# Optimization experiments

Measured on AMD Instinct MI355X. Metric: run time of the kernel, lower is better.

## Reference

```python
import jax, jax.numpy as jnp
import numpy as np

EPS = 1e-8       # module epsilon for L1 renormalize
LN_EPS = 1e-5    # torch LayerNorm default eps
NUM_ITER = 3
TEMP = 1.0


def _ln(x, g, b):
    m = x.mean(-1, keepdims=True)
    v = ((x - m) ** 2).mean(-1, keepdims=True)
    return (x - m) * jax.lax.rsqrt(v + LN_EPS) * g + b


def _gru(x, h, W_ih, W_hh, b_ih, b_hh):
    # torch GRUCell: r,z,n gate ordering
    gx = x @ W_ih.T + b_ih
    gh = h @ W_hh.T + b_hh
    xr, xz, xn = jnp.split(gx, 3, axis=-1)
    hr, hz, hn = jnp.split(gh, 3, axis=-1)
    r = jax.nn.sigmoid(xr + hr)
    z = jax.nn.sigmoid(xz + hz)
    n = jnp.tanh(xn + r * hn)
    return (1.0 - z) * n + z * h


def setup_inputs() -> dict:
    key = jax.random.key(0)
    ks = jax.random.split(key, 12)
    B, T, C, S, D, H = 32, 4096, 256, 8, 256, 512

    def xav(k, shape):
        fan_out, fan_in = shape
        lim = (6.0 / (fan_in + fan_out)) ** 0.5
        return jax.random.uniform(k, shape, jnp.float32, -lim, lim)

    return dict(
        inputs=jax.random.normal(ks[0], (B, T, C), jnp.float32),
        slots=jax.random.normal(ks[1], (B, S, D), jnp.float32),
        ln_in_g=jnp.ones((C,), jnp.float32), ln_in_b=jnp.zeros((C,), jnp.float32),
        ln_s_g=jnp.ones((D,), jnp.float32), ln_s_b=jnp.zeros((D,), jnp.float32),
        ln_m_g=jnp.ones((D,), jnp.float32), ln_m_b=jnp.zeros((D,), jnp.float32),
        Wq=xav(ks[2], (D, D)), Wk=xav(ks[3], (D, C)), Wv=xav(ks[4], (D, C)),
        W_ih=xav(ks[5], (3 * D, D)), W_hh=xav(ks[6], (3 * D, D)),
        b_ih=jnp.zeros((3 * D,), jnp.float32), b_hh=jnp.zeros((3 * D,), jnp.float32),
        W1=xav(ks[7], (H, D)), b1=jnp.zeros((H,), jnp.float32),
        W2=xav(ks[8], (D, H)), b2=jnp.zeros((D,), jnp.float32),
    )


def reference(inputs, slots, ln_in_g, ln_in_b, ln_s_g, ln_s_b, ln_m_g, ln_m_b,
              Wq, Wk, Wv, W_ih, W_hh, b_ih, b_hh, W1, b1, W2, b2):
    D = slots.shape[-1]
    x = _ln(inputs, ln_in_g, ln_in_b)           # [B,T,C]
    k = x @ Wk.T                                # [B,T,D]
    v = x @ Wv.T                                # [B,T,D]
    scale = D ** (-0.5)
    logits = attn_sw = None
    for _ in range(NUM_ITER):
        slots_prev = slots
        s = _ln(slots, ln_s_g, ln_s_b)
        q = (s @ Wq.T) * scale                  # [B,S,D]
        logits = jnp.einsum('bsd,btd->bst', q, k)
        attn = jax.nn.softmax(logits / TEMP, axis=1)   # softmax over slots
        a = attn + EPS
        attn_sw = a / a.sum(-1, keepdims=True)         # L1 renorm over tokens
        updates = jnp.einsum('bst,btd->bsd', attn_sw, v)
        slots = _gru(updates, slots_prev, W_ih, W_hh, b_ih, b_hh)
        slots = slots + (jax.nn.relu(_ln(slots, ln_m_g, ln_m_b) @ W1.T + b1) @ W2.T + b2)
    return slots, logits, attn_sw
```

## Files before the change

kernel.cpp:

```cpp
#include <hip/hip_runtime.h>
#include <cstdint>
#include <cstddef>

typedef __bf16 bf16;
typedef float  f32x4  __attribute__((ext_vector_type(4)));
typedef __bf16 bf16x8 __attribute__((ext_vector_type(8)));
typedef __bf16 bf16x4 __attribute__((ext_vector_type(4)));

__global__ __launch_bounds__(256) void k_prep1(
    const float* __restrict__ slots_in, const float* __restrict__ W1,
    const float* __restrict__ W2,
    float* __restrict__ slots, bf16* __restrict__ W1T, bf16* __restrict__ W2T)
{
    const int i = blockIdx.x * 256 + threadIdx.x;
    if      (i <  65536) { slots[i] = slots_in[i]; }
    else if (i < 196608) { int j = i -  65536; int k = j >> 9, c = j & 511;
                           W1T[j] = (bf16)W1[c*256 + k]; }
    else if (i < 327680) { int j = i - 196608; int k = j >> 8, c = j & 255;
                           W2T[j] = (bf16)W2[c*512 + k]; }
}

__global__ __launch_bounds__(256) void k_prep2(
    const float* __restrict__ Wq, const float* __restrict__ Wk,
    const float* __restrict__ W_ih, const float* __restrict__ Wv,
    bf16* __restrict__ Mqk, float* __restrict__ Wxg)
{
    const int c = threadIdx.x;
    __shared__ float v[256];
    if (blockIdx.x < 256) {
        const int e = blockIdx.x;
        v[c] = Wq[(size_t)c*256 + e];
        __syncthreads();
        float a = 0.f;
#pragma unroll 8
        for (int d = 0; d < 256; ++d) a += v[d] * Wk[(size_t)d*256 + c];
        Mqk[(size_t)e*256 + c] = (bf16)(a * 0.0625f);
    } else {
        const int g = blockIdx.x - 256;
        v[c] = W_ih[(size_t)g*256 + c];
        __syncthreads();
        float a = 0.f;
#pragma unroll 8
        for (int d = 0; d < 256; ++d) a += v[d] * Wv[(size_t)d*256 + c];
        Wxg[(size_t)g*256 + c] = a;
    }
}

__global__ __launch_bounds__(256) void k_prep3(
    const float* __restrict__ Wxg, const float* __restrict__ W_hh,
    bf16* __restrict__ WgT)
{
    const int j = blockIdx.x * 256 + threadIdx.x;
    const int k = j / 1536, col = j - k*1536;
    WgT[j] = (bf16)((col < 768) ? Wxg[(size_t)col*256 + k] : W_hh[(size_t)(col-768)*256 + k]);
}

__global__ __launch_bounds__(256) void k_ln_in(
    const float* __restrict__ x, const float* __restrict__ g,
    const float* __restrict__ b, bf16* __restrict__ xln)
{
    const int wave = threadIdx.x >> 6, lane = threadIdx.x & 63;
    const size_t row = (size_t)blockIdx.x * 4 + wave;
    const float* xr = x + row * 256 + lane * 4;
    f32x4 v = *(const f32x4*)xr;
    float s  = v[0] + v[1] + v[2] + v[3];
    float ss = v[0]*v[0] + v[1]*v[1] + v[2]*v[2] + v[3]*v[3];
#pragma unroll
    for (int m = 32; m >= 1; m >>= 1) { s += __shfl_xor(s, m); ss += __shfl_xor(ss, m); }
    const float mean = s * (1.f/256.f);
    const float var  = ss * (1.f/256.f) - mean*mean;
    const float rstd = rsqrtf(var + 1e-5f);
    const f32x4 gg = *(const f32x4*)(g + lane*4);
    const f32x4 bb = *(const f32x4*)(b + lane*4);
    bf16x4 o;
#pragma unroll
    for (int e = 0; e < 4; ++e) o[e] = (bf16)((v[e]-mean)*rstd*gg[e] + bb[e]);
    *(bf16x4*)(xln + row*256 + lane*4) = o;
}

__global__ __launch_bounds__(256) void k_tr(
    const bf16* __restrict__ xln, bf16* __restrict__ xlnT)
{
    const int tt = blockIdx.x, ct = blockIdx.y, b = blockIdx.z;
    const int tid = threadIdx.x;
    __shared__ __align__(16) char tile[64*128];
    {
        const int row = tid >> 2, cq = (tid & 3) * 16;
        const bf16* src = xln + ((size_t)(b*4096 + tt*64 + row))*256 + ct*64 + cq;
        bf16x8 v0 = *(const bf16x8*)src;
        bf16x8 v1 = *(const bf16x8*)(src + 8);
        const int swz = (row & 7) << 4;
        *(bf16x8*)(tile + row*128 + ((cq*2)      ^ swz)) = v0;
        *(bf16x8*)(tile + row*128 + ((cq*2 + 16) ^ swz)) = v1;
    }
    __syncthreads();
    {
        const int c = tid & 63, tq = tid >> 6;
        bf16 val[16];
#pragma unroll
        for (int j = 0; j < 16; ++j) {
            const int t = tq*16 + j;
            val[j] = *(const bf16*)(tile + t*128 + ((2*c) ^ ((t & 7) << 4)));
        }
        bf16* dst = xlnT + ((size_t)(b*256 + ct*64 + c))*4096 + tt*64 + tq*16;
        *(bf16x8*)dst       = *(bf16x8*)&val[0];
        *(bf16x8*)(dst + 8) = *(bf16x8*)&val[8];
    }
}

__device__ __forceinline__ void gemv8(const bf16* __restrict__ wp, int LDW,
                                      const float* __restrict__ sp, int klen4,
                                      float* __restrict__ ac)
{
#pragma unroll 8
    for (int k4 = 0; k4 < klen4; ++k4) {
        const f32x4 sv = *(const f32x4*)(sp + k4*4);
#pragma unroll
        for (int kk = 0; kk < 4; ++kk) {
            const bf16x8 w = *(const bf16x8*)(wp + (size_t)(k4*4+kk)*LDW);
#pragma unroll
            for (int j = 0; j < 8; ++j) ac[j] += sv[kk]*(float)w[j];
        }
    }
}

__global__ __launch_bounds__(256) void k_q0(
    const float* __restrict__ slots, const bf16* __restrict__ Mqk,
    const float* __restrict__ g_s, const float* __restrict__ b_s,
    bf16* __restrict__ q2bf, float* __restrict__ den)
{
    const int bs = blockIdx.x, tid = threadIdx.x;
    __shared__ float sln[256], part[2048], red[8];
    const float v0 = slots[(size_t)bs*256 + tid];
    if (tid == 0) den[bs] = 0.f;
    {
        float s1 = v0, s2 = v0*v0;
#pragma unroll
        for (int m = 32; m >= 1; m >>= 1) { s1 += __shfl_xor(s1, m); s2 += __shfl_xor(s2, m); }
        if ((tid & 63) == 0) { red[tid >> 6] = s1; red[4 + (tid >> 6)] = s2; }
    }
    __syncthreads();
    {
        const float mean = (red[0]+red[1]+red[2]+red[3])*(1.f/256.f);
        const float var  = (red[4]+red[5]+red[6]+red[7])*(1.f/256.f) - mean*mean;
        const float rstd = rsqrtf(var + 1e-5f);
        sln[tid] = (v0-mean)*rstd*g_s[tid] + b_s[tid];
    }
    __syncthreads();
    {
        const int g8 = tid & 31, ks = tid >> 5;
        float ac[8] = {0,0,0,0,0,0,0,0};
        gemv8(Mqk + (size_t)(ks*32)*256 + g8*8, 256, sln + ks*32, 8, ac);
#pragma unroll
        for (int j = 0; j < 8; ++j) part[ks*256 + g8*8 + j] = ac[j];
    }
    __syncthreads();
    {
        float a = 0.f;
#pragma unroll
        for (int k = 0; k < 8; ++k) a += part[k*256 + tid];
        q2bf[(size_t)bs*256 + tid] = (bf16)a;
    }
}

__global__ __launch_bounds__(256) void k_attn1(
    const bf16* __restrict__ xln, const bf16* __restrict__ q2bf,
    bf16* __restrict__ abuf, float* __restrict__ den,
    float* __restrict__ logits_out, int write_logits)
{
    const int chunk = blockIdx.x, b = blockIdx.y;
    const int wv = threadIdx.x >> 6, lane = threadIdx.x & 63;
    const int sA = lane & 15;
    const int ko = (lane >> 4) * 8;

    bf16x8 aq[8];
    if (sA < 8) {
#pragma unroll
        for (int kk = 0; kk < 8; ++kk)
            aq[kk] = *(const bf16x8*)(q2bf + (size_t)(b*8 + sA)*256 + kk*32 + ko);
    } else {
#pragma unroll
        for (int kk = 0; kk < 8; ++kk) aq[kk] = (bf16x8){0,0,0,0,0,0,0,0};
    }

    float dacc[4] = {0.f, 0.f, 0.f, 0.f};
#pragma unroll
    for (int it = 0; it < 4; ++it) {
        const int t0 = chunk*256 + wv*64 + it*16;
        f32x4 acc = {0.f, 0.f, 0.f, 0.f};
        const bf16* xp = xln + (size_t)(b*4096 + t0 + sA)*256 + ko;
#pragma unroll
        for (int kk = 0; kk < 8; ++kk) {
            const bf16x8 bfr = *(const bf16x8*)(xp + kk*32);
            acc = __builtin_amdgcn_mfma_f32_16x16x32_bf16(aq[kk], bfr, acc, 0, 0, 0);
        }
        if (lane < 32) {
            float m1 = fmaxf(fmaxf(acc[0], acc[1]), fmaxf(acc[2], acc[3]));
            const float m2 = __shfl_xor(m1, 16);
            const float mx = fmaxf(m1, m2);
            float e[4], s4 = 0.f;
#pragma unroll
            for (int r = 0; r < 4; ++r) { e[r] = expf(acc[r] - mx); s4 += e[r]; }
            const float so = __shfl_xor(s4, 16);
            const float inv = 1.f / (s4 + so);
            const int t = t0 + (lane & 15);
            bf16x4 ab;
#pragma unroll
            for (int r = 0; r < 4; ++r) {
                const float av = e[r]*inv + 1e-8f;
                dacc[r] += av;
                ab[r] = (bf16)av;
            }
            *(bf16x4*)(abuf + (size_t)(b*4096 + t)*8 + (lane >> 4)*4) = ab;
            if (write_logits) {
#pragma unroll
                for (int r = 0; r < 4; ++r)
                    logits_out[(size_t)(b*8 + (lane >> 4)*4 + r)*4096 + t] = acc[r];
            }
        }
    }
    if (lane < 32) {
#pragma unroll
        for (int r = 0; r < 4; ++r) {
            float v = dacc[r];
            v += __shfl_xor(v, 1); v += __shfl_xor(v, 2);
            v += __shfl_xor(v, 4); v += __shfl_xor(v, 8);
            if ((lane & 15) == 0) atomicAdd(&den[b*8 + (lane >> 4)*4 + r], v);
        }
    }
}

__global__ __launch_bounds__(256) void k_attn2(
    const bf16* __restrict__ xlnT, const bf16* __restrict__ abuf,
    float* __restrict__ numpart)
{
    const int chunk = blockIdx.x, b = blockIdx.y, tid = threadIdx.x;
    const int wv = tid >> 6, lane = tid & 63;
    __shared__ __align__(16) bf16 aT[8][528];

#pragma unroll
    for (int r = 0; r < 2; ++r) {
        const int t = r*256 + tid;
        const bf16x8 a8 = *(const bf16x8*)(abuf + ((size_t)b*4096 + chunk*512 + t)*8);
#pragma unroll
        for (int s = 0; s < 8; ++s) aT[s][t] = a8[s];
    }
    __syncthreads();

    const int sA = lane & 15, ko = (lane >> 4) * 8;
    f32x4 acc[4] = {{0,0,0,0},{0,0,0,0},{0,0,0,0},{0,0,0,0}};
#pragma unroll 4
    for (int kt = 0; kt < 16; ++kt) {
        bf16x8 af;
        if (sA < 8) af = *(const bf16x8*)&aT[sA][kt*32 + ko];
        else        af = (bf16x8){0,0,0,0,0,0,0,0};
#pragma unroll
        for (int i = 0; i < 4; ++i) {
            const int c = (wv + i*4)*16 + sA;
            const bf16x8 bfr = *(const bf16x8*)(
                xlnT + ((size_t)(b*256 + c))*4096 + chunk*512 + kt*32 + ko);
            acc[i] = __builtin_amdgcn_mfma_f32_16x16x32_bf16(af, bfr, acc[i], 0, 0, 0);
        }
    }
    if (lane < 32) {
#pragma unroll
        for (int i = 0; i < 4; ++i) {
            const int c = (wv + i*4)*16 + (lane & 15);
#pragma unroll
            for (int r = 0; r < 4; ++r) {
                const int s = (lane >> 4)*4 + r;
                numpart[(((size_t)b*8 + chunk)*8 + s)*256 + c] = acc[i][r];
            }
        }
    }
}

__global__ __launch_bounds__(256) void k_attnsw(
    const float* __restrict__ logits, const float* __restrict__ den,
    float* __restrict__ attn_out)
{
    const int chunk = blockIdx.x, b = blockIdx.y;
    const int t = chunk*256 + threadIdx.x;
    float l[8];
#pragma unroll
    for (int s = 0; s < 8; ++s) l[s] = logits[(size_t)(b*8 + s)*4096 + t];
    float mx = l[0];
#pragma unroll
    for (int s = 1; s < 8; ++s) mx = fmaxf(mx, l[s]);
    float e[8], sum = 0.f;
#pragma unroll
    for (int s = 0; s < 8; ++s) { e[s] = expf(l[s] - mx); sum += e[s]; }
    const float inv = 1.f/sum;
#pragma unroll
    for (int s = 0; s < 8; ++s)
        attn_out[(size_t)(b*8 + s)*4096 + t] = (e[s]*inv + 1e-8f) / den[b*8 + s];
}

__global__ __launch_bounds__(512) void k_slot(
    const float* __restrict__ numpart, float* __restrict__ den,
    float* __restrict__ slots,
    const bf16* __restrict__ WgT,
    const float* __restrict__ b_ih, const float* __restrict__ b_hh,
    const float* __restrict__ g_m, const float* __restrict__ b_m,
    const bf16* __restrict__ W1T, const float* __restrict__ b1,
    const bf16* __restrict__ W2T, const float* __restrict__ b2,
    const bf16* __restrict__ Mqk,
    const float* __restrict__ g_s, const float* __restrict__ b_s,
    bf16* __restrict__ q2bf, float* __restrict__ out_slots, int last)
{
    const int bs = blockIdx.x, b = bs >> 3, s = bs & 7;
    const int tid = threadIdx.x;
    __shared__ float HS[256], ynd[256], G[1536], hpr[256];
    __shared__ float hln[256], hid[512], sln[256];
    __shared__ float part[4096];
    __shared__ float red[8];
    __shared__ float dsc;

    {
        const int h = tid >> 8, d2 = tid & 255;
        float a = 0.f;
        const float* np = numpart + (((size_t)b*8 + h*4)*8 + s)*256 + d2;
#pragma unroll
        for (int c = 0; c < 4; ++c) a += np[(size_t)c*2048];
        part[h*256 + d2] = a;
        if (tid < 256) HS[tid] = slots[(size_t)bs*256 + tid];
        if (tid == 0) { dsc = den[bs]; den[bs] = 0.f; }
    }
    __syncthreads();
    if (tid < 256) ynd[tid] = (part[tid] + part[256 + tid]) / dsc;
    __syncthreads();

    if (tid < 384) {
        const int g8 = tid % 192, ks = tid / 192;
        const int col = g8*8;
        const float* sp = ((col < 768) ? ynd : HS) + ks*128;
        float ac[8] = {0,0,0,0,0,0,0,0};
        gemv8(WgT + (size_t)(ks*128)*1536 + col, 1536, sp, 32, ac);
#pragma unroll
        for (int j = 0; j < 8; ++j) part[ks*1536 + col + j] = ac[j];
    }
    __syncthreads();
    for (int t = tid; t < 1536; t += 512) {
        const float bias = (t < 768) ? b_ih[t] : b_hh[t - 768];
        G[t] = part[t] + part[1536 + t] + bias;
    }
    __syncthreads();

    if (tid < 256) {
        const float r = 1.f/(1.f + expf(-(G[tid]       + G[768  + tid])));
        const float z = 1.f/(1.f + expf(-(G[256 + tid] + G[1024 + tid])));
        const float n = tanhf(G[512 + tid] + r*G[1280 + tid]);
        hpr[tid] = (1.f - z)*n + z*HS[tid];
    }
    __syncthreads();

    if (tid < 256) {
        const float v = hpr[tid];
        float s1 = v, s2 = v*v;
#pragma unroll
        for (int m = 32; m >= 1; m >>= 1) { s1 += __shfl_xor(s1, m); s2 += __shfl_xor(s2, m); }
        if ((tid & 63) == 0) { red[tid >> 6] = s1; red[4 + (tid >> 6)] = s2; }
    }
    __syncthreads();
    if (tid < 256) {
        const float mean = (red[0]+red[1]+red[2]+red[3])*(1.f/256.f);
        const float var  = (red[4]+red[5]+red[6]+red[7])*(1.f/256.f) - mean*mean;
        const float rstd = rsqrtf(var + 1e-5f);
        hln[tid] = (hpr[tid]-mean)*rstd*g_m[tid] + b_m[tid];
    }
    __syncthreads();

    {
        const int g8 = tid & 63, ks = tid >> 6;
        float ac[8] = {0,0,0,0,0,0,0,0};
        gemv8(W1T + (size_t)(ks*32)*512 + g8*8, 512, hln + ks*32, 8, ac);
#pragma unroll
        for (int j = 0; j < 8; ++j) part[ks*512 + g8*8 + j] = ac[j];
    }
    __syncthreads();
    {
        float a = b1[tid];
#pragma unroll
        for (int k = 0; k < 8; ++k) a += part[k*512 + tid];
        hid[tid] = fmaxf(a, 0.f);
    }
    __syncthreads();

    {
        const int g8 = tid & 31, ks = tid >> 5;
        float ac[8] = {0,0,0,0,0,0,0,0};
        gemv8(W2T + (size_t)(ks*32)*256 + g8*8, 256, hid + ks*32, 8, ac);
#pragma unroll
        for (int j = 0; j < 8; ++j) part[ks*256 + g8*8 + j] = ac[j];
    }
    __syncthreads();
    if (tid < 256) {
        float a = 0.f;
#pragma unroll
        for (int k = 0; k < 16; ++k) a += part[k*256 + tid];
        const float val = hpr[tid] + a + b2[tid];
        HS[tid] = val;
        slots[(size_t)bs*256 + tid] = val;
        if (last) out_slots[(size_t)bs*256 + tid] = val;
    }
    __syncthreads();
    if (last) return;

    if (tid < 256) {
        const float v = HS[tid];
        float s1 = v, s2 = v*v;
#pragma unroll
        for (int m = 32; m >= 1; m >>= 1) { s1 += __shfl_xor(s1, m); s2 += __shfl_xor(s2, m); }
        if ((tid & 63) == 0) { red[tid >> 6] = s1; red[4 + (tid >> 6)] = s2; }
    }
    __syncthreads();
    if (tid < 256) {
        const float mean = (red[0]+red[1]+red[2]+red[3])*(1.f/256.f);
        const float var  = (red[4]+red[5]+red[6]+red[7])*(1.f/256.f) - mean*mean;
        const float rstd = rsqrtf(var + 1e-5f);
        sln[tid] = (HS[tid]-mean)*rstd*g_s[tid] + b_s[tid];
    }
    __syncthreads();

    {
        const int g8 = tid & 31, ks = tid >> 5;
        float ac[8] = {0,0,0,0,0,0,0,0};
        gemv8(Mqk + (size_t)(ks*16)*256 + g8*8, 256, sln + ks*16, 4, ac);
#pragma unroll
        for (int j = 0; j < 8; ++j) part[ks*256 + g8*8 + j] = ac[j];
    }
    __syncthreads();
    if (tid < 256) {
        float a = 0.f;
#pragma unroll
        for (int k = 0; k < 16; ++k) a += part[k*256 + tid];
        q2bf[(size_t)bs*256 + tid] = (bf16)a;
    }
}

extern "C" void kernel_launch(void* const* d_in, const int* in_sizes, int n_in,
                              void* d_out, int out_size, void* d_ws, size_t ws_size,
                              hipStream_t stream)
{
    const float* x        = (const float*)d_in[0];
    const float* slots_in = (const float*)d_in[1];
    const float* ln_in_g  = (const float*)d_in[2];
    const float* ln_in_b  = (const float*)d_in[3];
    const float* ln_s_g   = (const float*)d_in[4];
    const float* ln_s_b   = (const float*)d_in[5];
    const float* ln_m_g   = (const float*)d_in[6];
    const float* ln_m_b   = (const float*)d_in[7];
    const float* Wq       = (const float*)d_in[8];
    const float* Wk       = (const float*)d_in[9];
    const float* Wv       = (const float*)d_in[10];
    const float* W_ih     = (const float*)d_in[11];
    const float* W_hh     = (const float*)d_in[12];
    const float* b_ih     = (const float*)d_in[13];
    const float* b_hh     = (const float*)d_in[14];
    const float* W1       = (const float*)d_in[15];
    const float* b1       = (const float*)d_in[16];
    const float* W2       = (const float*)d_in[17];
    const float* b2       = (const float*)d_in[18];

    float* out_slots  = (float*)d_out;
    float* out_logits = out_slots + 65536;
    float* out_attn   = out_logits + 1048576;

    char* w = (char*)d_ws;
    bf16*  xln     = (bf16*)w;   w += 67108864;
    bf16*  xlnT    = (bf16*)w;   w += 67108864;
    bf16*  q2bf    = (bf16*)w;   w += 131072;
    bf16*  abuf    = (bf16*)w;   w += 2097152;
    float* slots   = (float*)w;  w += 262144;
    bf16*  WgT     = (bf16*)w;   w += 786432;
    bf16*  W1T     = (bf16*)w;   w += 262144;
    bf16*  W2T     = (bf16*)w;   w += 262144;
    bf16*  Mqk     = (bf16*)w;   w += 131072;
    float* Wxg     = (float*)w;  w += 786432;
    float* numpart = (float*)w;  w += 2097152;
    float* den     = (float*)w;  w += 4096;
    if ((size_t)(w - (char*)d_ws) > ws_size) return;

    k_prep1<<<1280, 256, 0, stream>>>(slots_in, W1, W2, slots, W1T, W2T);
    k_prep2<<<1024, 256, 0, stream>>>(Wq, Wk, W_ih, Wv, Mqk, Wxg);
    k_prep3<<<1536, 256, 0, stream>>>(Wxg, W_hh, WgT);
    k_ln_in<<<32768, 256, 0, stream>>>(x, ln_in_g, ln_in_b, xln);
    k_tr<<<dim3(64, 4, 32), 256, 0, stream>>>(xln, xlnT);
    k_q0<<<256, 256, 0, stream>>>(slots, Mqk, ln_s_g, ln_s_b, q2bf, den);

    for (int it = 0; it < 3; ++it) {
        const int last = (it == 2);
        k_attn1<<<dim3(16, 32), 256, 0, stream>>>(xln, q2bf, abuf, den, out_logits, last);
        k_attn2<<<dim3(8, 32), 256, 0, stream>>>(xlnT, abuf, numpart);
        if (last)
            k_attnsw<<<dim3(16, 32), 256, 0, stream>>>(out_logits, den, out_attn);
        k_slot<<<256, 512, 0, stream>>>(numpart, den, slots,
                                        WgT, b_ih, b_hh,
                                        ln_m_g, ln_m_b, W1T, b1, W2T, b2,
                                        Mqk, ln_s_g, ln_s_b,
                                        q2bf, out_slots, last);
    }
}
```

Before: 305.1 us.

## Fuse input LayerNorm with transpose and split attn2 into more chunks

The input LayerNorm and the separate transpose kernel are merged into one kernel. Each block normalizes 64 token rows, writes the row-major bf16 result, and transposes the tile through swizzled shared memory to produce xlnT, so xln no longer has to be re-read from global memory. Separately, the k_attn2 token chunk shrinks from 512 to 256 and the grid doubles to 16x32, giving more blocks to fill the GPU. This doubles the numpart partial-sum buffer and the number of reductions k_slot performs. The fused kernel holds 64 floats per thread in registers and has each thread do 64 scalar LDS reads, which may limit occupancy.

```diff
diff --git a/kernel.cpp b/kernel.cpp
--- a/kernel.cpp
+++ b/kernel.cpp
@@ -55,56 +55,58 @@
     WgT[j] = (bf16)((col < 768) ? Wxg[(size_t)col*256 + k] : W_hh[(size_t)(col-768)*256 + k]);
 }
 
-__global__ __launch_bounds__(256) void k_ln_in(
+__global__ __launch_bounds__(256) void k_lnt(
     const float* __restrict__ x, const float* __restrict__ g,
-    const float* __restrict__ b, bf16* __restrict__ xln)
-{
-    const int wave = threadIdx.x >> 6, lane = threadIdx.x & 63;
-    const size_t row = (size_t)blockIdx.x * 4 + wave;
-    const float* xr = x + row * 256 + lane * 4;
-    f32x4 v = *(const f32x4*)xr;
-    float s  = v[0] + v[1] + v[2] + v[3];
-    float ss = v[0]*v[0] + v[1]*v[1] + v[2]*v[2] + v[3]*v[3];
-#pragma unroll
-    for (int m = 32; m >= 1; m >>= 1) { s += __shfl_xor(s, m); ss += __shfl_xor(ss, m); }
-    const float mean = s * (1.f/256.f);
-    const float var  = ss * (1.f/256.f) - mean*mean;
+    const float* __restrict__ b, bf16* __restrict__ xln, bf16* __restrict__ xlnT)
+{
+    const int tt = blockIdx.x, bb = blockIdx.y, tid = threadIdx.x;
+    __shared__ __align__(16) char tile[64*512];
+    const int row = tid >> 2, q = tid & 3;
+    const size_t grow = (size_t)(bb*4096 + tt*64 + row);
+
+    f32x4 v[16];
+    const float* xr = x + grow*256 + q*64;
+#pragma unroll
+    for (int i = 0; i < 16; ++i) v[i] = *(const f32x4*)(xr + i*4);
+    float s1 = 0.f, s2 = 0.f;
+#pragma unroll
+    for (int i = 0; i < 16; ++i) {
+#pragma unroll
+        for (int e = 0; e < 4; ++e) { s1 += v[i][e]; s2 += v[i][e]*v[i][e]; }
+    }
+    s1 += __shfl_xor(s1, 1); s2 += __shfl_xor(s2, 1);
+    s1 += __shfl_xor(s1, 2); s2 += __shfl_xor(s2, 2);
+    const float mean = s1 * (1.f/256.f);
+    const float var  = s2 * (1.f/256.f) - mean*mean;
     const float rstd = rsqrtf(var + 1e-5f);
-    const f32x4 gg = *(const f32x4*)(g + lane*4);
-    const f32x4 bb = *(const f32x4*)(b + lane*4);
-    bf16x4 o;
-#pragma unroll
-    for (int e = 0; e < 4; ++e) o[e] = (bf16)((v[e]-mean)*rstd*gg[e] + bb[e]);
-    *(bf16x4*)(xln + row*256 + lane*4) = o;
-}
-
-__global__ __launch_bounds__(256) void k_tr(
-    const bf16* __restrict__ xln, bf16* __restrict__ xlnT)
-{
-    const int tt = blockIdx.x, ct = blockIdx.y, b = blockIdx.z;
-    const int tid = threadIdx.x;
-    __shared__ __align__(16) char tile[64*128];
-    {
-        const int row = tid >> 2, cq = (tid & 3) * 16;
-        const bf16* src = xln + ((size_t)(b*4096 + tt*64 + row))*256 + ct*64 + cq;
-        bf16x8 v0 = *(const bf16x8*)src;
-        bf16x8 v1 = *(const bf16x8*)(src + 8);
-        const int swz = (row & 7) << 4;
-        *(bf16x8*)(tile + row*128 + ((cq*2)      ^ swz)) = v0;
-        *(bf16x8*)(tile + row*128 + ((cq*2 + 16) ^ swz)) = v1;
-    }
-    __syncthreads();
-    {
-        const int c = tid & 63, tq = tid >> 6;
-        bf16 val[16];
-#pragma unroll
-        for (int j = 0; j < 16; ++j) {
-            const int t = tq*16 + j;
-            val[j] = *(const bf16*)(tile + t*128 + ((2*c) ^ ((t & 7) << 4)));
-        }
-        bf16* dst = xlnT + ((size_t)(b*256 + ct*64 + c))*4096 + tt*64 + tq*16;
-        *(bf16x8*)dst       = *(bf16x8*)&val[0];
-        *(bf16x8*)(dst + 8) = *(bf16x8*)&val[8];
+
+    const int swz = (row & 7) << 4;
+#pragma unroll
+    for (int i = 0; i < 8; ++i) {
+        const int cbase = q*64 + i*8;
+        const f32x4 g0 = *(const f32x4*)(g + cbase), g1 = *(const f32x4*)(g + cbase + 4);
+        const f32x4 b0 = *(const f32x4*)(b + cbase), b1 = *(const f32x4*)(b + cbase + 4);
+        bf16x8 o;
+#pragma unroll
+        for (int e = 0; e < 4; ++e) {
+            o[e]   = (bf16)((v[i*2][e]   - mean)*rstd*g0[e] + b0[e]);
+            o[4+e] = (bf16)((v[i*2+1][e] - mean)*rstd*g1[e] + b1[e]);
+        }
+        *(bf16x8*)(xln + grow*256 + cbase) = o;
+        *(bf16x8*)(tile + row*512 + ((cbase*2) ^ swz)) = o;
+    }
+    __syncthreads();
+
+    {
+        const int c = tid;
+        bf16 val[64];
+#pragma unroll
+        for (int t = 0; t < 64; ++t)
+            val[t] = *(const bf16*)(tile + t*512 + ((2*c) ^ ((t & 7) << 4)));
+        bf16* dst = xlnT + ((size_t)(bb*256 + c))*4096 + tt*64;
+#pragma unroll
+        for (int i = 0; i < 8; ++i)
+            *(bf16x8*)(dst + i*8) = *(bf16x8*)&val[i*8];
     }
 }
 
@@ -236,21 +238,19 @@
 {
     const int chunk = blockIdx.x, b = blockIdx.y, tid = threadIdx.x;
     const int wv = tid >> 6, lane = tid & 63;
-    __shared__ __align__(16) bf16 aT[8][528];
-
-#pragma unroll
-    for (int r = 0; r < 2; ++r) {
-        const int t = r*256 + tid;
-        const bf16x8 a8 = *(const bf16x8*)(abuf + ((size_t)b*4096 + chunk*512 + t)*8);
-#pragma unroll
-        for (int s = 0; s < 8; ++s) aT[s][t] = a8[s];
+    __shared__ __align__(16) bf16 aT[8][272];
+
+    {
+        const bf16x8 a8 = *(const bf16x8*)(abuf + ((size_t)b*4096 + chunk*256 + tid)*8);
+#pragma unroll
+        for (int s = 0; s < 8; ++s) aT[s][tid] = a8[s];
     }
     __syncthreads();
 
     const int sA = lane & 15, ko = (lane >> 4) * 8;
     f32x4 acc[4] = {{0,0,0,0},{0,0,0,0},{0,0,0,0},{0,0,0,0}};
-#pragma unroll 4
-    for (int kt = 0; kt < 16; ++kt) {
+#pragma unroll
+    for (int kt = 0; kt < 8; ++kt) {
         bf16x8 af;
         if (sA < 8) af = *(const bf16x8*)&aT[sA][kt*32 + ko];
         else        af = (bf16x8){0,0,0,0,0,0,0,0};
@@ -258,7 +258,7 @@
         for (int i = 0; i < 4; ++i) {
             const int c = (wv + i*4)*16 + sA;
             const bf16x8 bfr = *(const bf16x8*)(
-                xlnT + ((size_t)(b*256 + c))*4096 + chunk*512 + kt*32 + ko);
+                xlnT + ((size_t)(b*256 + c))*4096 + chunk*256 + kt*32 + ko);
             acc[i] = __builtin_amdgcn_mfma_f32_16x16x32_bf16(af, bfr, acc[i], 0, 0, 0);
         }
     }
@@ -269,7 +269,7 @@
 #pragma unroll
             for (int r = 0; r < 4; ++r) {
                 const int s = (lane >> 4)*4 + r;
-                numpart[(((size_t)b*8 + chunk)*8 + s)*256 + c] = acc[i][r];
+                numpart[(((size_t)b*16 + chunk)*8 + s)*256 + c] = acc[i][r];
             }
         }
     }
@@ -319,9 +319,9 @@
     {
         const int h = tid >> 8, d2 = tid & 255;
         float a = 0.f;
-        const float* np = numpart + (((size_t)b*8 + h*4)*8 + s)*256 + d2;
-#pragma unroll
-        for (int c = 0; c < 4; ++c) a += np[(size_t)c*2048];
+        const float* np = numpart + (((size_t)b*16 + h*8)*8 + s)*256 + d2;
+#pragma unroll
+        for (int c = 0; c < 8; ++c) a += np[(size_t)c*2048];
         part[h*256 + d2] = a;
         if (tid < 256) HS[tid] = slots[(size_t)bs*256 + tid];
         if (tid == 0) { dsc = den[bs]; den[bs] = 0.f; }
@@ -477,21 +477,20 @@
     bf16*  W2T     = (bf16*)w;   w += 262144;
     bf16*  Mqk     = (bf16*)w;   w += 131072;
     float* Wxg     = (float*)w;  w += 786432;
-    float* numpart = (float*)w;  w += 2097152;
+    float* numpart = (float*)w;  w += 4194304;
     float* den     = (float*)w;  w += 4096;
     if ((size_t)(w - (char*)d_ws) > ws_size) return;
 
     k_prep1<<<1280, 256, 0, stream>>>(slots_in, W1, W2, slots, W1T, W2T);
     k_prep2<<<1024, 256, 0, stream>>>(Wq, Wk, W_ih, Wv, Mqk, Wxg);
     k_prep3<<<1536, 256, 0, stream>>>(Wxg, W_hh, WgT);
-    k_ln_in<<<32768, 256, 0, stream>>>(x, ln_in_g, ln_in_b, xln);
-    k_tr<<<dim3(64, 4, 32), 256, 0, stream>>>(xln, xlnT);
+    k_lnt<<<dim3(64, 32), 256, 0, stream>>>(x, ln_in_g, ln_in_b, xln, xlnT);
     k_q0<<<256, 256, 0, stream>>>(slots, Mqk, ln_s_g, ln_s_b, q2bf, den);
 
     for (int it = 0; it < 3; ++it) {
         const int last = (it == 2);
         k_attn1<<<dim3(16, 32), 256, 0, stream>>>(xln, q2bf, abuf, den, out_logits, last);
-        k_attn2<<<dim3(8, 32), 256, 0, stream>>>(xlnT, abuf, numpart);
+        k_attn2<<<dim3(16, 32), 256, 0, stream>>>(xlnT, abuf, numpart);
         if (last)
             k_attnsw<<<dim3(16, 32), 256, 0, stream>>>(out_logits, den, out_attn);
         k_slot<<<256, 512, 0, stream>>>(numpart, den, slots,
```

After: 349.3 us. +14.5%, slower.
